# Kernel tuning notes

Hardware: AMD Instinct MI355X
Metric: run time of the kernel (lower is better)

The kernel has to match this reference:

```python
import jax, jax.numpy as jnp
import numpy as np

K = 20
EPS = 1e-5


def _knn_idx(x, k):
    # x: [B, N, D] -> indices of k nearest neighbors per node (self included,
    # matching torch_cluster.knn(x, x, k)).
    sq = jnp.sum(x * x, axis=-1)                      # [B, N]
    d = sq[:, :, None] + sq[:, None, :] - 2.0 * jnp.einsum('bnd,bmd->bnm', x, x)
    return jax.lax.top_k(-d, k)[1]                    # [B, N, k]


def _edge_feat(x, idx):
    # EdgeConv edge feature: concat(x_i, x_j - x_i)  -> [B, N, k, 2D]
    xj = jax.vmap(lambda xb, ib: xb[ib])(x, idx)      # [B, N, k, D]
    xi = jnp.broadcast_to(x[:, :, None, :], xj.shape)
    return jnp.concatenate([xi, xj - xi], axis=-1)


def _bn(h, g, b):
    # training-mode batch norm over all edges (PyG MLP default norm)
    mean = jnp.mean(h, axis=(0, 1, 2), keepdims=True)
    var = jnp.var(h, axis=(0, 1, 2), keepdims=True)
    return g * (h - mean) * jax.lax.rsqrt(var + EPS) + b


def _lin_init(key, fin, fout):
    k1, k2 = jax.random.split(key)
    s = 1.0 / np.sqrt(fin)
    W = jax.random.uniform(k1, (fin, fout), jnp.float32, -s, s)
    b = jax.random.uniform(k2, (fout,), jnp.float32, -s, s)
    return W, b


def setup_inputs() -> dict:
    key = jax.random.key(0)
    ks = jax.random.split(key, 8)
    B, N = 32, 1024
    pos = jax.random.normal(ks[0], (B, N, 3), jnp.float32)
    W1, b1 = _lin_init(ks[1], 6, 64)
    W2, b2 = _lin_init(ks[2], 64, 64)
    W3, b3 = _lin_init(ks[3], 64, 64)
    Wc2, bc2 = _lin_init(ks[4], 128, 128)
    Wl, bl = _lin_init(ks[5], 192, 1024)
    Wm1, bm1 = _lin_init(ks[6], 1024, 512)
    Wm2, bm2 = _lin_init(ks[7], 512, 256)
    Wm3, bm3 = _lin_init(jax.random.fold_in(key, 99), 256, 40)
    g1 = jnp.ones((64,), jnp.float32); be1 = jnp.zeros((64,), jnp.float32)
    g2 = jnp.ones((64,), jnp.float32); be2 = jnp.zeros((64,), jnp.float32)
    return dict(pos=pos, W1=W1, b1=b1, g1=g1, be1=be1, W2=W2, b2=b2, g2=g2,
                be2=be2, W3=W3, b3=b3, Wc2=Wc2, bc2=bc2, Wl=Wl, bl=bl,
                Wm1=Wm1, bm1=bm1, Wm2=Wm2, bm2=bm2, Wm3=Wm3, bm3=bm3)


def reference(pos, W1, b1, g1, be1, W2, b2, g2, be2, W3, b3, Wc2, bc2,
              Wl, bl, Wm1, bm1, Wm2, bm2, Wm3, bm3):
    # DynamicEdgeConv 1: kNN in coordinate space, MLP [6,64,64,64] (plain last)
    e1 = _edge_feat(pos, _knn_idx(pos, K))            # [B, N, k, 6]
    h = jax.nn.relu(_bn(e1 @ W1 + b1, g1, be1))
    h = jax.nn.relu(_bn(h @ W2 + b2, g2, be2))
    h = h @ W3 + b3
    x1 = jnp.max(h, axis=2)                           # [B, N, 64] max aggr
    # DynamicEdgeConv 2: kNN in feature space, single plain Linear 128->128
    e2 = _edge_feat(x1, _knn_idx(x1, K))              # [B, N, k, 128]
    x2 = jnp.max(e2 @ Wc2 + bc2, axis=2)              # [B, N, 128]
    # linear + global max pool + head MLP (norm=None, dropout=identity/eval)
    lin = jnp.concatenate([x1, x2], axis=-1) @ Wl + bl  # [B, N, 1024]
    pooled = jnp.max(lin, axis=1)                     # [B, 1024]
    h = jax.nn.relu(pooled @ Wm1 + bm1)
    h = jax.nn.relu(h @ Wm2 + bm2)
    return h @ Wm3 + bm3                              # [B, 40]
```

## Files before the change

### kernel.cpp

```cpp
#include <hip/hip_runtime.h>
#include <hip/hip_bf16.h>
#include <float.h>
#include <math.h>

typedef __hip_bfloat16 bf16;
typedef unsigned long long u64;

#define BATCH 32
#define NPTS  1024
#define KNN   20
#define NB    (BATCH*NPTS)
#define NEDGE (NB*KNN)

#define OFF_FLAG 512u
#define OFF_INB  1024u
#define OFF_IDX  988928u
#define OFF_X1   1644288u
#define OFF_X2   3741440u
#define OFF_C1   5838592u
#define OFF_POOL 7935744u
#define SLOW_END 8066816u
#define OFF_B2H  8066816u
#define FAST_END 10163968u
#define IN_POSF 0u
#define IN_B1   98304u
#define IN_G1   98368u
#define IN_BE1  98432u
#define IN_B2   98496u
#define IN_G2   98560u
#define IN_BE2  98624u
#define IN_B3   98688u
#define IN_BC2  98752u
#define IN_BL   98880u
#define IN_BM1  99904u
#define IN_BM2  100416u
#define IN_BM3  100672u
#define IN_W1   100736u
#define IN_WBUF 101120u
#define WB_W2   0u
#define WB_W3   4096u
#define WB_WD   8192u
#define WB_WBOT 16384u
#define WB_WL   24576u
#define WB_WM1  221184u
#define WB_WM2  745472u
#define WB_WM3  876544u
#define IN_TOTAL 987904u

__device__ __forceinline__ float bf2f(bf16 v){ return __bfloat162float(v); }

__device__ __forceinline__ unsigned int mono32(float f){
  unsigned int b = __float_as_uint(f);
  return b ^ ((unsigned int)((int)b >> 31) | 0x80000000u);
}

typedef __attribute__((ext_vector_type(8))) short bf16x8;
typedef __attribute__((ext_vector_type(4))) float f32x4;

__device__ __forceinline__ unsigned short bfhi(float f){
  unsigned int u = __float_as_uint(f);
  u += 0x7FFFu + ((u >> 16) & 1u);
  return (unsigned short)(u >> 16);
}
__device__ __forceinline__ void bfsplit(float f, unsigned short& h, unsigned short& l){
  h = bfhi(f);
  float fh = __uint_as_float(((unsigned int)h) << 16);
  l = bfhi(f - fh);
}

#define REP20(M) M(0) M(1) M(2) M(3) M(4) M(5) M(6) M(7) M(8) M(9) \
                 M(10) M(11) M(12) M(13) M(14) M(15) M(16) M(17) M(18) M(19)
#define SH19(M) M(19,18) M(18,17) M(17,16) M(16,15) M(15,14) M(14,13) M(13,12) \
                M(12,11) M(11,10) M(10,9) M(9,8) M(8,7) M(7,6) M(6,5) M(5,4) \
                M(4,3) M(3,2) M(2,1) M(1,0)

__device__ __forceinline__ double packkey(float d, int idx){
  unsigned int b = __float_as_uint(fmaxf(d, 0.0f));
  u64 k = 0x4000000000000000ULL | ((u64)b << 20) | (unsigned int)idx;
  return __longlong_as_double((long long)k);
}

#define KDECLD(p) double rk##p = DBL_MAX;
#define KMM(p,pm) rk##p = fmin(rk##p, fmax(rk##pm, _k));
#define INS_MM(kv) do{ double _k=(kv); SH19(KMM) rk0 = fmin(rk0, _k); }while(0)

#define KPUB_A(p) mrgA[q_l*21+p] = (u64)__double_as_longlong(rk##p);
#define KPUB_B(p) mrgB[q_l*21+p] = (u64)__double_as_longlong(rk##p);
#define KSTG(p)   gpart[p] = (u64)__double_as_longlong(rk##p);
#define KLDAD(p)  double rk##p = __longlong_as_double((long long)pa[p]);
#define KOUTU(p)  optr[p] = (int)((u64)__double_as_longlong(rk##p) & 1023ULL);

__global__ void k_sniff(const void* pos_raw, int* flag){
  if (blockIdx.x == 0 && threadIdx.x == 0){
    const unsigned short* h = (const unsigned short*)pos_raw;
    int wild = 0;
    for (int k = 0; k < 16; k++){
      unsigned int bits = ((unsigned int)h[2*k]) << 16;
      float v = __uint_as_float(bits);
      float a = fabsf(v);
      if (a != 0.0f && (v != v || a > 1e10f || a < 1e-10f)) wild++;
    }
    *flag = (wild >= 4) ? 1 : 0;
  }
}

__device__ __forceinline__ float rdv(const void* p, int i, int f){
  return f ? ((const float*)p)[i] : bf2f(((const bf16*)p)[i]);
}

__global__ __launch_bounds__(256) void k_cvt(
    const void* pos, const void* W1, const void* b1, const void* g1, const void* be1,
    const void* W2, const void* b2, const void* g2, const void* be2,
    const void* W3, const void* b3, const void* Wc2, const void* bc2,
    const void* Wl, const void* bl, const void* Wm1, const void* bm1,
    const void* Wm2, const void* bm2, const void* Wm3, const void* bm3,
    const int* flag, float* inb){
  int id = blockIdx.x*256 + threadIdx.x;
  if (id >= (int)IN_TOTAL) return;
  int f = *flag;
  float v;
  if      (id < 98304)  v = rdv(pos, id, f);
  else if (id < 98368)  v = rdv(b1,  id-98304, f);
  else if (id < 98432)  v = rdv(g1,  id-98368, f);
  else if (id < 98496)  v = rdv(be1, id-98432, f);
  else if (id < 98560)  v = rdv(b2,  id-98496, f);
  else if (id < 98624)  v = rdv(g2,  id-98560, f);
  else if (id < 98688)  v = rdv(be2, id-98624, f);
  else if (id < 98752)  v = rdv(b3,  id-98688, f);
  else if (id < 98880)  v = rdv(bc2, id-98752, f);
  else if (id < 99904)  v = rdv(bl,  id-98880, f);
  else if (id < 100416) v = rdv(bm1, id-99904, f);
  else if (id < 100672) v = rdv(bm2, id-100416, f);
  else if (id < 100712) v = rdv(bm3, id-100672, f);
  else if (id < 100736) v = 0.0f;
  else if (id < 101120) v = rdv(W1,  id-100736, f);
  else {
    int t = id - 101120;
    if      (t < 4096)   v = rdv(W2, t, f);
    else if (t < 8192)   v = rdv(W3, t-4096, f);
    else if (t < 16384){ int u = t-8192;  v = rdv(Wc2, u, f) - rdv(Wc2, 8192+u, f); }
    else if (t < 24576){ int u = t-16384; v = rdv(Wc2, 8192+u, f); }
    else if (t < 221184) v = rdv(Wl,  t-24576, f);
    else if (t < 745472){ int u = t-221184; int c = u>>10, d = u&1023; v = rdv(Wm1, d*512+c, f); }
    else if (t < 876544){ int u = t-745472; int c = u>>9,  d = u&511;  v = rdv(Wm2, d*256+c, f); }
    else               { int u = t-876544; int c = u>>8,  d = u&255;  v = rdv(Wm3, d*40+c, f); }
  }
  inb[id] = v;
}

__global__ __launch_bounds__(256) void k_prep1(const float* inb, float* a1, float* c1){
  const float* posf = inb + IN_POSF;
  const float* W1f  = inb + IN_W1;
  const float* b1f  = inb + IN_B1;
  int id = blockIdx.x*256 + threadIdx.x;
  int bn = id >> 6, c = id & 63;
  float p0 = posf[bn*3], p1 = posf[bn*3+1], p2 = posf[bn*3+2];
  float wt0 = W1f[c],     wt1 = W1f[64+c],  wt2 = W1f[128+c];
  float wb0 = W1f[192+c], wb1 = W1f[256+c], wb2 = W1f[320+c];
  float cv = p0*wb0 + p1*wb1 + p2*wb2;
  float av = p0*(wt0-wb0) + p1*(wt1-wb1) + p2*(wt2-wb2) + b1f[c];
  a1[id] = av;  c1[id] = cv;
}

__global__ __launch_bounds__(256, 2) void k_knn1(const float* inb, u64* part){
  const float* posf = inb + IN_POSF;
  __shared__ __align__(16) char sm1[21504];
  float* psx = (float*)sm1;
  float* psy = psx + 1024;
  float* psz = psy + 1024;
  float* sqs = psz + 1024;
  u64* mrgA = (u64*)sm1;
  u64* mrgB = (u64*)(sm1 + 10752);
  int bb   = blockIdx.x >> 5;
  int qg   = (blockIdx.x >> 1) & 15;
  int half = blockIdx.x & 1;
  int tid = threadIdx.x;
  int q_l = tid & 63;
  int slot = tid >> 6;
  for (int t = tid; t < 1024; t += 256){
    float x = posf[(bb*1024+t)*3], y = posf[(bb*1024+t)*3+1], z = posf[(bb*1024+t)*3+2];
    psx[t] = x; psy[t] = y; psz[t] = z; sqs[t] = x*x + y*y + z*z;
  }
  __syncthreads();
  int i_l = qg*64 + q_l;
  float xi0 = psx[i_l], xi1 = psy[i_l], xi2 = psz[i_l];
  float sqi = sqs[i_l];
  REP20(KDECLD)
  int cbase = half*512;
  for (int u = 0; u < 128; u++){
    int jj = cbase + 4*u + slot;
    float dot = xi0*psx[jj] + xi1*psy[jj] + xi2*psz[jj];
    float d = sqi + sqs[jj] - 2.0f*dot;
    INS_MM(packkey(d, jj));
  }
  __syncthreads();
  if (slot == 1){ REP20(KPUB_A) }
  if (slot == 3){ REP20(KPUB_B) }
  __syncthreads();
  if ((slot & 1) == 0){
    const u64* src = (slot == 0) ? &mrgA[q_l*21] : &mrgB[q_l*21];
    for (int p = 0; p < KNN; p++){
      double kv = __longlong_as_double((long long)src[p]);
      if (kv > rk19) break;
      INS_MM(kv);
    }
  }
  __syncthreads();
  if (slot == 2){ REP20(KPUB_B) }
  __syncthreads();
  if (slot == 0){
    const u64* src = &mrgB[q_l*21];
    for (int p = 0; p < KNN; p++){
      double kv = __longlong_as_double((long long)src[p]);
      if (kv > rk19) break;
      INS_MM(kv);
    }
    int gi = bb*1024 + i_l;
    u64* gpart = part + ((size_t)gi*2 + half)*KNN;
    REP20(KSTG)
  }
}

__global__ __launch_bounds__(256) void k_mrg(const u64* part, int* out){
  int gi = blockIdx.x*256 + threadIdx.x;
  const u64* pa = part + (size_t)gi*2*KNN;
  REP20(KLDAD)
  for (int p = 0; p < KNN; p++){
    double kv = __longlong_as_double((long long)pa[KNN + p]);
    if (kv > rk19) break;
    INS_MM(kv);
  }
  int* optr = out + gi*KNN;
  REP20(KOUTU)
}

__global__ __launch_bounds__(256) void k_stats1(const float* a1, const float* c1,
                                                const int* idx1, double* stats){
  __shared__ float rs[256], rs2[256];
  int tid = threadIdx.x, c = tid & 63, slot = tid >> 6;
  int base = blockIdx.x * 1024;
  float s = 0.f, s2 = 0.f;
  for (int t = 0; t < 256; t++){
    unsigned e = (unsigned)(base + t*4 + slot);
    int i = (int)(e / 20u);
    int b = i >> 10;
    int j = idx1[e];
    float h = a1[i*64+c] + c1[((b<<10)+j)*64 + c];
    s += h; s2 += h*h;
  }
  rs[tid] = s; rs2[tid] = s2;
  __syncthreads();
  if (slot == 0){
    double ts  = (double)rs[c]  + (double)rs[64+c]  + (double)rs[128+c]  + (double)rs[192+c];
    double ts2 = (double)rs2[c] + (double)rs2[64+c] + (double)rs2[128+c] + (double)rs2[192+c];
    atomicAdd(&stats[c], ts);
    atomicAdd(&stats[64+c], ts2);
  }
}


__global__ __launch_bounds__(256) void k_stats2m(const float* a1, const float* c1,
    const int* idx1, const float* inb, double* stats){
  __shared__ __align__(16) float W2s[4096];
  __shared__ float sc1s[64], sh1s[64];
  __shared__ float rs[4][64], rs2[4][64];
  int tid = threadIdx.x;
  const float* wbuf = inb + IN_WBUF;
  for (int t = tid; t < 4096; t += 256) W2s[t] = wbuf[WB_W2 + t];
  if (tid < 64){
    int c = tid;
    const double M = (double)NEDGE;
    double m1 = stats[c]/M;
    double v1 = stats[64+c]/M - m1*m1;
    double r1 = 1.0/sqrt(v1 + 1e-5);
    double g1 = (double)inb[IN_G1 + c];
    sc1s[c] = (float)(g1*r1);
    sh1s[c] = (float)((double)inb[IN_BE1 + c] - m1*g1*r1);
  }
  __syncthreads();
  int lane = tid & 63, wv = tid >> 6;
  int c16 = lane & 15, ag = lane >> 4, kb0 = ag*8;
  bf16x8 w2h[4][2], w2l[4][2];
  #pragma unroll
  for (int nt = 0; nt < 4; nt++){
    #pragma unroll
    for (int ks = 0; ks < 2; ks++){
      bf16x8 h8, l8;
      #pragma unroll
      for (int e = 0; e < 8; e++){
        unsigned short hh, ll;
        bfsplit(W2s[(ks*32 + kb0 + e)*64 + nt*16 + c16], hh, ll);
        h8[e] = (short)hh; l8[e] = (short)ll;
      }
      w2h[nt][ks] = h8; w2l[nt][ks] = l8;
    }
  }
  float sa[4] = {0,0,0,0}, qa[4] = {0,0,0,0};
  for (int t4 = 0; t4 < 4; t4++){
    int T = t4*4 + wv;
    int node_l = T >> 1, half = T & 1;
    int nodeg = blockIdx.x*8 + node_l;
    int krow = half*16 + c16;
    int rr = (krow < 20);
    int j = idx1[nodeg*20 + (rr ? krow : 0)];
    int gj = ((nodeg >> 10) << 10) + j;
    const float* ar = a1 + (size_t)nodeg*64;
    const float* cr = c1 + (size_t)gj*64;
    f32x4 av0 = *(const f32x4*)(ar + kb0);
    f32x4 av1 = *(const f32x4*)(ar + kb0 + 4);
    f32x4 av2 = *(const f32x4*)(ar + 32 + kb0);
    f32x4 av3 = *(const f32x4*)(ar + 36 + kb0);
    f32x4 cv0 = *(const f32x4*)(cr + kb0);
    f32x4 cv1 = *(const f32x4*)(cr + kb0 + 4);
    f32x4 cv2 = *(const f32x4*)(cr + 32 + kb0);
    f32x4 cv3 = *(const f32x4*)(cr + 36 + kb0);
    bf16x8 a0h, a0l, a1h_, a1l_;
    #pragma unroll
    for (int e = 0; e < 4; e++){
      unsigned short hh, ll;
      float h;
      h = rr ? fmaxf((av0[e]+cv0[e])*sc1s[kb0+e] + sh1s[kb0+e], 0.f) : 0.f;
      bfsplit(h, hh, ll); a0h[e] = (short)hh; a0l[e] = (short)ll;
      h = rr ? fmaxf((av1[e]+cv1[e])*sc1s[kb0+4+e] + sh1s[kb0+4+e], 0.f) : 0.f;
      bfsplit(h, hh, ll); a0h[4+e] = (short)hh; a0l[4+e] = (short)ll;
      h = rr ? fmaxf((av2[e]+cv2[e])*sc1s[32+kb0+e] + sh1s[32+kb0+e], 0.f) : 0.f;
      bfsplit(h, hh, ll); a1h_[e] = (short)hh; a1l_[e] = (short)ll;
      h = rr ? fmaxf((av3[e]+cv3[e])*sc1s[36+kb0+e] + sh1s[36+kb0+e], 0.f) : 0.f;
      bfsplit(h, hh, ll); a1h_[4+e] = (short)hh; a1l_[4+e] = (short)ll;
    }
    #pragma unroll
    for (int nt = 0; nt < 4; nt++){
      f32x4 acc = {0.f, 0.f, 0.f, 0.f};
      acc = __builtin_amdgcn_mfma_f32_16x16x32_bf16(a0h,  w2h[nt][0], acc, 0, 0, 0);
      acc = __builtin_amdgcn_mfma_f32_16x16x32_bf16(a1h_, w2h[nt][1], acc, 0, 0, 0);
      acc = __builtin_amdgcn_mfma_f32_16x16x32_bf16(a0h,  w2l[nt][0], acc, 0, 0, 0);
      acc = __builtin_amdgcn_mfma_f32_16x16x32_bf16(a1h_, w2l[nt][1], acc, 0, 0, 0);
      acc = __builtin_amdgcn_mfma_f32_16x16x32_bf16(a0l,  w2h[nt][0], acc, 0, 0, 0);
      acc = __builtin_amdgcn_mfma_f32_16x16x32_bf16(a1l_, w2h[nt][1], acc, 0, 0, 0);
      #pragma unroll
      for (int r = 0; r < 4; r++){
        int kr = half*16 + 4*ag + r;
        float v = (kr < 20) ? acc[r] : 0.f;
        sa[nt] += v; qa[nt] += v*v;
      }
    }
  }
  #pragma unroll
  for (int nt = 0; nt < 4; nt++){
    sa[nt] += __shfl_xor(sa[nt], 16); sa[nt] += __shfl_xor(sa[nt], 32);
    qa[nt] += __shfl_xor(qa[nt], 16); qa[nt] += __shfl_xor(qa[nt], 32);
  }
  if (ag == 0){
    #pragma unroll
    for (int nt = 0; nt < 4; nt++){
      rs[wv][nt*16+c16] = sa[nt];
      rs2[wv][nt*16+c16] = qa[nt];
    }
  }
  __syncthreads();
  if (tid < 64){
    double ts = (double)rs[0][tid] + (double)rs[1][tid]
              + (double)rs[2][tid] + (double)rs[3][tid];
    double tq = (double)rs2[0][tid] + (double)rs2[1][tid]
              + (double)rs2[2][tid] + (double)rs2[3][tid];
    atomicAdd(&stats[128+tid], ts);
    atomicAdd(&stats[192+tid], tq);
  }
}

__global__ __launch_bounds__(256, 2) void k_x1m(const float* a1, const float* c1,
    const int* idx1, const float* inb, const double* stats, float* x1){
  __shared__ __align__(16) unsigned short W2hF[4096], W2lF[4096];
  __shared__ __align__(16) unsigned short W3hF[4096], W3lF[4096];
  __shared__ __align__(16) float scr[4][16*68];
  __shared__ unsigned int mxp[4][8][64];
  __shared__ float sc1s[64], sh1s[64], sc2s[64], sh2s[64];
  int tid = threadIdx.x;
  const float* wbuf = inb + IN_WBUF;
  for (int t = tid; t < 4096; t += 256){
    int nt = t >> 10, ks = (t >> 9) & 1, ln = (t >> 3) & 63, e = t & 7;
    int row = ks*32 + (ln >> 4)*8 + e;
    int col = nt*16 + (ln & 15);
    unsigned short hh, ll;
    bfsplit(wbuf[WB_W2 + row*64 + col], hh, ll);
    W2hF[t] = hh; W2lF[t] = ll;
    bfsplit(wbuf[WB_W3 + row*64 + col], hh, ll);
    W3hF[t] = hh; W3lF[t] = ll;
  }
  {
    unsigned int* mf = &mxp[0][0][0];
    for (int t = tid; t < 2048; t += 256) mf[t] = 0u;
  }
  if (tid < 64){
    int c = tid;
    const double M = (double)NEDGE;
    double m1 = stats[c]/M;
    double v1 = stats[64+c]/M - m1*m1;
    double r1 = 1.0/sqrt(v1 + 1e-5);
    double g1 = (double)inb[IN_G1 + c];
    sc1s[c] = (float)(g1*r1);
    sh1s[c] = (float)((double)inb[IN_BE1 + c] - m1*g1*r1);
    double mp = stats[128+c]/M;
    double v2 = stats[192+c]/M - mp*mp;
    double r2 = 1.0/sqrt(v2 + 1e-5);
    double g2 = (double)inb[IN_G2 + c];
    sc2s[c] = (float)(g2*r2);
    sh2s[c] = (float)((double)inb[IN_BE2 + c] - mp*g2*r2);
  }
  __syncthreads();
  int lane = tid & 63, wv = tid >> 6;
  int c16 = lane & 15, ag = lane >> 4, kb0 = ag*8;
  float scn[4], shn[4];
  #pragma unroll
  for (int nt = 0; nt < 4; nt++){
    scn[nt] = sc2s[nt*16 + c16];
    shn[nt] = sh2s[nt*16 + c16];
  }
  float* sw = &scr[wv][0];
  for (int t4 = 0; t4 < 4; t4++){
    int T = t4*4 + wv;
    int node_l = T >> 1, half = T & 1;
    int nodeg = blockIdx.x*8 + node_l;
    int krow = half*16 + c16;
    int rr = (krow < 20);
    int j = idx1[nodeg*20 + (rr ? krow : 0)];
    int gj = ((nodeg >> 10) << 10) + j;
    const float* ar = a1 + (size_t)nodeg*64;
    const float* cr = c1 + (size_t)gj*64;
    f32x4 av0 = *(const f32x4*)(ar + kb0);
    f32x4 av1 = *(const f32x4*)(ar + kb0 + 4);
    f32x4 av2 = *(const f32x4*)(ar + 32 + kb0);
    f32x4 av3 = *(const f32x4*)(ar + 36 + kb0);
    f32x4 cv0 = *(const f32x4*)(cr + kb0);
    f32x4 cv1 = *(const f32x4*)(cr + kb0 + 4);
    f32x4 cv2 = *(const f32x4*)(cr + 32 + kb0);
    f32x4 cv3 = *(const f32x4*)(cr + 36 + kb0);
    bf16x8 a0h, a0l, a1h_, a1l_;
    #pragma unroll
    for (int e = 0; e < 4; e++){
      unsigned short hh, ll;
      float h;
      h = rr ? fmaxf((av0[e]+cv0[e])*sc1s[kb0+e] + sh1s[kb0+e], 0.f) : 0.f;
      bfsplit(h, hh, ll); a0h[e] = (short)hh; a0l[e] = (short)ll;
      h = rr ? fmaxf((av1[e]+cv1[e])*sc1s[kb0+4+e] + sh1s[kb0+4+e], 0.f) : 0.f;
      bfsplit(h, hh, ll); a0h[4+e] = (short)hh; a0l[4+e] = (short)ll;
      h = rr ? fmaxf((av2[e]+cv2[e])*sc1s[32+kb0+e] + sh1s[32+kb0+e], 0.f) : 0.f;
      bfsplit(h, hh, ll); a1h_[e] = (short)hh; a1l_[e] = (short)ll;
      h = rr ? fmaxf((av3[e]+cv3[e])*sc1s[36+kb0+e] + sh1s[36+kb0+e], 0.f) : 0.f;
      bfsplit(h, hh, ll); a1h_[4+e] = (short)hh; a1l_[4+e] = (short)ll;
    }
    f32x4 pacc[4];
    #pragma unroll
    for (int nt = 0; nt < 4; nt++){
      bf16x8 wh0 = *(const bf16x8*)(W2hF + (nt*2+0)*512 + lane*8);
      bf16x8 wh1 = *(const bf16x8*)(W2hF + (nt*2+1)*512 + lane*8);
      bf16x8 wl0 = *(const bf16x8*)(W2lF + (nt*2+0)*512 + lane*8);
      bf16x8 wl1 = *(const bf16x8*)(W2lF + (nt*2+1)*512 + lane*8);
      f32x4 acc = {0.f, 0.f, 0.f, 0.f};
      acc = __builtin_amdgcn_mfma_f32_16x16x32_bf16(a0h,  wh0, acc, 0, 0, 0);
      acc = __builtin_amdgcn_mfma_f32_16x16x32_bf16(a1h_, wh1, acc, 0, 0, 0);
      acc = __builtin_amdgcn_mfma_f32_16x16x32_bf16(a0h,  wl0, acc, 0, 0, 0);
      acc = __builtin_amdgcn_mfma_f32_16x16x32_bf16(a1h_, wl1, acc, 0, 0, 0);
      acc = __builtin_amdgcn_mfma_f32_16x16x32_bf16(a0l,  wh0, acc, 0, 0, 0);
      acc = __builtin_amdgcn_mfma_f32_16x16x32_bf16(a1l_, wh1, acc, 0, 0, 0);
      pacc[nt] = acc;
    }
    #pragma unroll
    for (int nt = 0; nt < 4; nt++){
      #pragma unroll
      for (int r = 0; r < 4; r++){
        float v = fmaxf(pacc[nt][r]*scn[nt] + shn[nt], 0.f);
        sw[(4*ag + r)*68 + nt*16 + c16] = v;
      }
    }
    f32x4 h20 = *(const f32x4*)(sw + c16*68 + kb0);
    f32x4 h21 = *(const f32x4*)(sw + c16*68 + kb0 + 4);
    f32x4 h22 = *(const f32x4*)(sw + c16*68 + 32 + kb0);
    f32x4 h23 = *(const f32x4*)(sw + c16*68 + 36 + kb0);
    bf16x8 b0h, b0l, b1h, b1l;
    #pragma unroll
    for (int e = 0; e < 4; e++){
      unsigned short hh, ll;
      bfsplit(h20[e], hh, ll); b0h[e] = (short)hh; b0l[e] = (short)ll;
      bfsplit(h21[e], hh, ll); b0h[4+e] = (short)hh; b0l[4+e] = (short)ll;
      bfsplit(h22[e], hh, ll); b1h[e] = (short)hh; b1l[e] = (short)ll;
      bfsplit(h23[e], hh, ll); b1h[4+e] = (short)hh; b1l[4+e] = (short)ll;
    }
    #pragma unroll
    for (int nt = 0; nt < 4; nt++){
      bf16x8 wh0 = *(const bf16x8*)(W3hF + (nt*2+0)*512 + lane*8);
      bf16x8 wh1 = *(const bf16x8*)(W3hF + (nt*2+1)*512 + lane*8);
      bf16x8 wl0 = *(const bf16x8*)(W3lF + (nt*2+0)*512 + lane*8);
      bf16x8 wl1 = *(const bf16x8*)(W3lF + (nt*2+1)*512 + lane*8);
      f32x4 acc = {0.f, 0.f, 0.f, 0.f};
      acc = __builtin_amdgcn_mfma_f32_16x16x32_bf16(b0h, wh0, acc, 0, 0, 0);
      acc = __builtin_amdgcn_mfma_f32_16x16x32_bf16(b1h, wh1, acc, 0, 0, 0);
      acc = __builtin_amdgcn_mfma_f32_16x16x32_bf16(b0h, wl0, acc, 0, 0, 0);
      acc = __builtin_amdgcn_mfma_f32_16x16x32_bf16(b1h, wl1, acc, 0, 0, 0);
      acc = __builtin_amdgcn_mfma_f32_16x16x32_bf16(b0l, wh0, acc, 0, 0, 0);
      acc = __builtin_amdgcn_mfma_f32_16x16x32_bf16(b1l, wh1, acc, 0, 0, 0);
      float vmx = -FLT_MAX;
      #pragma unroll
      for (int r = 0; r < 4; r++){
        int kr = half*16 + 4*ag + r;
        vmx = (kr < 20) ? fmaxf(vmx, acc[r]) : vmx;
      }
      vmx = fmaxf(vmx, __shfl_xor(vmx, 16));
      vmx = fmaxf(vmx, __shfl_xor(vmx, 32));
      if (ag == 0){
        unsigned int u = mono32(vmx);
        unsigned int* sl = &mxp[wv][node_l][nt*16 + c16];
        if (u > *sl) *sl = u;
      }
    }
  }
  __syncthreads();
  for (int s = tid; s < 512; s += 256){
    int nl = s >> 6, c = s & 63;
    unsigned int u = mxp[0][nl][c];
    unsigned int u1 = mxp[1][nl][c]; u = (u1 > u) ? u1 : u;
    unsigned int u2 = mxp[2][nl][c]; u = (u2 > u) ? u2 : u;
    unsigned int u3 = mxp[3][nl][c]; u = (u3 > u) ? u3 : u;
    unsigned int bts = (u & 0x80000000u) ? (u ^ 0x80000000u) : ~u;
    x1[(size_t)(blockIdx.x*8 + nl)*64 + c] = __uint_as_float(bts) + inb[IN_B3 + c];
  }
}

__global__ __launch_bounds__(256, 4) void k_knn2(const float* x1, u64* part){
  __shared__ __align__(16) char sm2[35584];
  unsigned short* Ch = (unsigned short*)sm2;
  unsigned short* Cl = (unsigned short*)(sm2 + 9216);
  float* Dd  = (float*)(sm2 + 18432);
  float* sqc = (float*)(sm2 + 35072);
  float* sqq = (float*)(sm2 + 35328);
  u64* mrgA = (u64*)sm2;
  u64* mrgB = (u64*)(sm2 + 10752);
  int bb   = blockIdx.x >> 5;
  int qg   = (blockIdx.x >> 1) & 15;
  int half = blockIdx.x & 1;
  int tid = threadIdx.x;
  int q_l = tid & 63;
  int wv = tid >> 6;
  int lane = tid & 63;
  int c16 = lane & 15, ag = lane >> 4, kb0 = ag*8;
  int qbase = bb*1024 + qg*64;
  bf16x8 qh0, qh1, ql0, ql1;
  {
    const float* qr = x1 + (size_t)(qbase + wv*16 + c16)*64;
    f32x4 v0 = *(const f32x4*)(qr + kb0);
    f32x4 v1 = *(const f32x4*)(qr + kb0 + 4);
    f32x4 v2 = *(const f32x4*)(qr + 32 + kb0);
    f32x4 v3 = *(const f32x4*)(qr + 36 + kb0);
    #pragma unroll
    for (int e = 0; e < 4; e++){
      unsigned short hh, ll;
      bfsplit(v0[e], hh, ll); qh0[e] = (short)hh; ql0[e] = (short)ll;
      bfsplit(v1[e], hh, ll); qh0[4+e] = (short)hh; ql0[4+e] = (short)ll;
      bfsplit(v2[e], hh, ll); qh1[e] = (short)hh; ql1[e] = (short)ll;
      bfsplit(v3[e], hh, ll); qh1[4+e] = (short)hh; ql1[4+e] = (short)ll;
    }
  }
  if (tid < 64){
    const float* xr = x1 + (size_t)(qbase + tid)*64;
    float s = 0.f;
    #pragma unroll
    for (int d4 = 0; d4 < 16; d4++){
      f32x4 v = *(const f32x4*)(xr + d4*4);
      s += v[0]*v[0] + v[1]*v[1] + v[2]*v[2] + v[3]*v[3];
    }
    sqq[tid] = s;
  }
  REP20(KDECLD)
  for (int ch = 0; ch < 8; ch++){
    int c0 = half*512 + ch*64;
    __syncthreads();
    for (int pp = tid; pp < 2048; pp += 256){
      int row = pp >> 5, cp = pp & 31;
      const float* src = x1 + (size_t)(bb*1024 + c0 + row)*64 + cp*2;
      float v0 = src[0], v1 = src[1];
      unsigned short h0, l0, h1, l1;
      bfsplit(v0, h0, l0); bfsplit(v1, h1, l1);
      ((unsigned int*)Ch)[row*36 + cp] = (unsigned int)h0 | ((unsigned int)h1 << 16);
      ((unsigned int*)Cl)[row*36 + cp] = (unsigned int)l0 | ((unsigned int)l1 << 16);
    }
    __syncthreads();
    if (tid < 64){
      float s = 0.f;
      for (int dw = 0; dw < 32; dw++){
        unsigned int hw = ((unsigned int*)Ch)[tid*36 + dw];
        unsigned int lw = ((unsigned int*)Cl)[tid*36 + dw];
        float a0 = __uint_as_float(hw << 16) + __uint_as_float(lw << 16);
        float a1 = __uint_as_float(hw & 0xFFFF0000u) + __uint_as_float(lw & 0xFFFF0000u);
        s += a0*a0 + a1*a1;
      }
      sqc[tid] = s;
    }
    __syncthreads();
    #pragma unroll
    for (int nt = 0; nt < 4; nt++){
      bf16x8 bh0 = *(const bf16x8*)(Ch + (nt*16 + c16)*72 + kb0);
      bf16x8 bh1 = *(const bf16x8*)(Ch + (nt*16 + c16)*72 + 32 + kb0);
      bf16x8 bl0 = *(const bf16x8*)(Cl + (nt*16 + c16)*72 + kb0);
      bf16x8 bl1 = *(const bf16x8*)(Cl + (nt*16 + c16)*72 + 32 + kb0);
      f32x4 p0 = {0.f,0.f,0.f,0.f}, p1 = {0.f,0.f,0.f,0.f}, p2 = {0.f,0.f,0.f,0.f};
      p0 = __builtin_amdgcn_mfma_f32_16x16x32_bf16(qh0, bh0, p0, 0, 0, 0);
      p0 = __builtin_amdgcn_mfma_f32_16x16x32_bf16(qh1, bh1, p0, 0, 0, 0);
      p1 = __builtin_amdgcn_mfma_f32_16x16x32_bf16(qh0, bl0, p1, 0, 0, 0);
      p1 = __builtin_amdgcn_mfma_f32_16x16x32_bf16(qh1, bl1, p1, 0, 0, 0);
      p2 = __builtin_amdgcn_mfma_f32_16x16x32_bf16(ql0, bh0, p2, 0, 0, 0);
      p2 = __builtin_amdgcn_mfma_f32_16x16x32_bf16(ql1, bh1, p2, 0, 0, 0);
      #pragma unroll
      for (int r = 0; r < 4; r++){
        int qrow = wv*16 + 4*ag + r;
        float d = sqq[qrow] + sqc[nt*16 + c16] - 2.0f*(p0[r] + p1[r] + p2[r]);
        Dd[qrow*65 + nt*16 + c16] = d;
      }
    }
    __syncthreads();
    for (int u = 0; u < 16; u += 2){
      int cA = 4*u + wv, cB = 4*(u+1) + wv;
      float dA = Dd[q_l*65 + cA];
      float dB = Dd[q_l*65 + cB];
      INS_MM(packkey(dA, c0 + cA));
      INS_MM(packkey(dB, c0 + cB));
    }
  }
  __syncthreads();
  if (wv == 1){ REP20(KPUB_A) }
  if (wv == 3){ REP20(KPUB_B) }
  __syncthreads();
  if ((wv & 1) == 0){
    const u64* src = (wv == 0) ? &mrgA[q_l*21] : &mrgB[q_l*21];
    for (int p = 0; p < KNN; p++){
      double kv = __longlong_as_double((long long)src[p]);
      if (kv > rk19) break;
      INS_MM(kv);
    }
  }
  __syncthreads();
  if (wv == 2){ REP20(KPUB_B) }
  __syncthreads();
  if (wv == 0){
    const u64* src = &mrgB[q_l*21];
    for (int p = 0; p < KNN; p++){
      double kv = __longlong_as_double((long long)src[p]);
      if (kv > rk19) break;
      INS_MM(kv);
    }
    int gi = qbase + q_l;
    u64* gpart = part + ((size_t)gi*2 + half)*KNN;
    REP20(KSTG)
  }
}

__global__ __launch_bounds__(256) void k_B2h(const float* x1, const float* inb,
                                             int q, float* B2H){
  __shared__ __align__(16) float Wbh[4096];
  __shared__ __align__(16) float xsh[1024];
  int tid = threadIdx.x;
  const float* Wb = inb + IN_WBUF + WB_WBOT;
  for (int t = tid; t < 4096; t += 256){
    int r = t >> 6, cl = t & 63;
    Wbh[t] = Wb[r*128 + q*64 + cl];
  }
  int node0 = blockIdx.x * 16;
  for (int t = tid; t < 1024; t += 256) xsh[t] = x1[node0*64 + t];
  __syncthreads();
  int n_l = tid >> 4, cg = tid & 15;
  const float* xr = xsh + n_l*64;
  float4 acc = make_float4(0.f,0.f,0.f,0.f);
  #pragma unroll 8
  for (int d = 0; d < 64; d++){
    float v = xr[d];
    float4 w = *(const float4*)(Wbh + d*64 + cg*4);
    acc.x += v*w.x; acc.y += v*w.y; acc.z += v*w.z; acc.w += v*w.w;
  }
  *(float4*)(B2H + (node0 + n_l)*64 + cg*4) = acc;
}

__global__ __launch_bounds__(256) void k_x2h(const float* x1, const float* B2H,
                                             const float* inb, const int* idx2,
                                             int q, float* x2){
  __shared__ __align__(16) float Wdh[4096];
  __shared__ __align__(16) float xsh[256];
  int tid = threadIdx.x;
  const float* Wd = inb + IN_WBUF + WB_WD;
  for (int t = tid; t < 4096; t += 256){
    int r = t >> 6, cl = t & 63;
    Wdh[t] = Wd[r*128 + q*64 + cl];
  }
  int node0 = blockIdx.x * 4;
  xsh[tid] = x1[node0*64 + tid];
  __syncthreads();
  int n_l = tid >> 6, cl = tid & 63;
  int i = node0 + n_l;
  int b = i >> 10;
  const float* xr = xsh + n_l*64;
  float acc = inb[IN_BC2 + q*64 + cl];
  #pragma unroll 8
  for (int d = 0; d < 64; d++) acc += xr[d]*Wdh[d*64 + cl];
  float m = -FLT_MAX;
  for (int kk = 0; kk < KNN; kk++){
    int j = idx2[i*KNN + kk];
    m = fmaxf(m, B2H[((b<<10)+j)*64 + cl]);
  }
  x2[i*128 + q*64 + cl] = acc + m;
}

__global__ __launch_bounds__(256) void k_x2d(const float* x1, const float* inb,
                                             const int* idx2, float* x2){
  __shared__ __align__(16) float Wdh[4096], Wbh[4096];
  __shared__ __align__(16) float xis[1024], xjs[1024];
  int tid = threadIdx.x;
  int q = blockIdx.x & 1;
  int node0 = (blockIdx.x >> 1) * 16;
  const float* Wd = inb + IN_WBUF + WB_WD;
  const float* Wb = inb + IN_WBUF + WB_WBOT;
  for (int t = tid; t < 4096; t += 256){
    int r = t >> 6, cl = t & 63;
    Wdh[t] = Wd[r*128 + q*64 + cl];
    Wbh[t] = Wb[r*128 + q*64 + cl];
  }
  for (int t = tid; t < 1024; t += 256) xis[t] = x1[node0*64 + t];
  __syncthreads();
  int n_l = tid >> 4, cg = tid & 15;
  int i = node0 + n_l, b = i >> 10;
  const float* xr = xis + n_l*64;
  float4 af = make_float4(inb[IN_BC2 + q*64 + cg*4],   inb[IN_BC2 + q*64 + cg*4+1],
                          inb[IN_BC2 + q*64 + cg*4+2], inb[IN_BC2 + q*64 + cg*4+3]);
  #pragma unroll 8
  for (int d = 0; d < 64; d++){
    float v = xr[d];
    float4 w = *(const float4*)(Wdh + d*64 + cg*4);
    af.x += v*w.x; af.y += v*w.y; af.z += v*w.z; af.w += v*w.w;
  }
  float4 mx = make_float4(-FLT_MAX,-FLT_MAX,-FLT_MAX,-FLT_MAX);
  for (int kk = 0; kk < KNN; kk++){
    __syncthreads();
    for (int t = tid; t < 1024; t += 256){
      int nn = t >> 6, r = t & 63;
      int jj = idx2[(node0+nn)*KNN + kk];
      xjs[t] = x1[((((node0+nn) >> 10) << 10) + jj)*64 + r];
    }
    __syncthreads();
    const float* xj = xjs + n_l*64;
    float4 acc = make_float4(0.f,0.f,0.f,0.f);
    #pragma unroll 8
    for (int d = 0; d < 64; d++){
      float v = xj[d];
      float4 w = *(const float4*)(Wbh + d*64 + cg*4);
      acc.x += v*w.x; acc.y += v*w.y; acc.z += v*w.z; acc.w += v*w.w;
    }
    mx.x = fmaxf(mx.x, acc.x); mx.y = fmaxf(mx.y, acc.y);
    mx.z = fmaxf(mx.z, acc.z); mx.w = fmaxf(mx.w, acc.w);
  }
  *(float4*)(x2 + i*128 + q*64 + cg*4) =
      make_float4(af.x+mx.x, af.y+mx.y, af.z+mx.z, af.w+mx.w);
}

__global__ __launch_bounds__(512, 2) void k_linpoolm(const float* x1, const float* x2,
    const float* inb, float* pool4){
  __shared__ __align__(16) float F[16*196];
  int tid = threadIdx.x;
  int b = blockIdx.x >> 4, cq = (blockIdx.x >> 2) & 3, nh = blockIdx.x & 3;
  int lane = tid & 63, wv = tid >> 6;
  int c16 = lane & 15, ag = lane >> 4;
  const float* Wl = inb + IN_WBUF + WB_WL;
  bf16x8 w_h[2][6], w_l[2][6];
  #pragma unroll
  for (int nt = 0; nt < 2; nt++){
    int col = cq*256 + (wv*2+nt)*16 + c16;
    #pragma unroll
    for (int ks = 0; ks < 6; ks++){
      bf16x8 h8, l8;
      #pragma unroll
      for (int e = 0; e < 8; e++){
        unsigned short hh, ll;
        bfsplit(Wl[(ks*32 + ag*8 + e)*1024 + col], hh, ll);
        h8[e] = (short)hh; l8[e] = (short)ll;
      }
      w_h[nt][ks] = h8; w_l[nt][ks] = l8;
    }
  }
  float rmax[2] = {-FLT_MAX, -FLT_MAX};
  int n0 = b*1024 + nh*256;
  for (int chk = 0; chk < 16; chk++){
    int nb = n0 + chk*16;
    __syncthreads();
    {
      int row = tid >> 5;
      int d0 = (tid & 31)*6;
      #pragma unroll
      for (int u = 0; u < 6; u++){
        int d = d0 + u;
        F[row*196 + d] = (d < 64) ? x1[(size_t)(nb+row)*64 + d]
                                  : x2[(size_t)(nb+row)*128 + d - 64];
      }
    }
    __syncthreads();
    bf16x8 a_h[6], a_l[6];
    #pragma unroll
    for (int ks = 0; ks < 6; ks++){
      f32x4 v0 = *(const f32x4*)(F + c16*196 + ks*32 + ag*8);
      f32x4 v1 = *(const f32x4*)(F + c16*196 + ks*32 + ag*8 + 4);
      bf16x8 h8, l8;
      #pragma unroll
      for (int e = 0; e < 4; e++){
        unsigned short hh, ll;
        bfsplit(v0[e], hh, ll); h8[e] = (short)hh; l8[e] = (short)ll;
        bfsplit(v1[e], hh, ll); h8[4+e] = (short)hh; l8[4+e] = (short)ll;
      }
      a_h[ks] = h8; a_l[ks] = l8;
    }
    #pragma unroll
    for (int nt = 0; nt < 2; nt++){
      f32x4 p0 = {0.f,0.f,0.f,0.f}, p1 = {0.f,0.f,0.f,0.f}, p2 = {0.f,0.f,0.f,0.f};
      #pragma unroll
      for (int ks = 0; ks < 6; ks++){
        p0 = __builtin_amdgcn_mfma_f32_16x16x32_bf16(a_h[ks], w_h[nt][ks], p0, 0, 0, 0);
        p1 = __builtin_amdgcn_mfma_f32_16x16x32_bf16(a_h[ks], w_l[nt][ks], p1, 0, 0, 0);
        p2 = __builtin_amdgcn_mfma_f32_16x16x32_bf16(a_l[ks], w_h[nt][ks], p2, 0, 0, 0);
      }
      float m = -FLT_MAX;
      #pragma unroll
      for (int r = 0; r < 4; r++) m = fmaxf(m, p0[r] + p1[r] + p2[r]);
// ... 143 lines not shown
```

Measured before the change: 820.9 us.

## Pack edges densely into MFMA tiles to drop padded rows in stats2 and x1

Each node previously had 20 edges spread over two 16-row MFMA tiles, so 12 of every 32 rows were padding. The kernels now pack a block's 160 edges contiguously into 10 full 16-row tiles, with tiles that straddle two nodes split into two max reductions merged by shared-memory atomicMax. stats2m also stops building the W2 hi/lo fragments in registers and reads pre-split fragments from shared memory, as x1m already did. This cuts MFMA and gather work by about a fifth, at the cost of idle waves in the last round (10 tiles over 4 waves) and LDS atomics.

```diff
diff --git a/kernel.cpp b/kernel.cpp
--- a/kernel.cpp
+++ b/kernel.cpp
@@ -261,12 +261,19 @@
 
 __global__ __launch_bounds__(256) void k_stats2m(const float* a1, const float* c1,
     const int* idx1, const float* inb, double* stats){
-  __shared__ __align__(16) float W2s[4096];
+  __shared__ __align__(16) unsigned short W2hF[4096], W2lF[4096];
   __shared__ float sc1s[64], sh1s[64];
   __shared__ float rs[4][64], rs2[4][64];
   int tid = threadIdx.x;
   const float* wbuf = inb + IN_WBUF;
-  for (int t = tid; t < 4096; t += 256) W2s[t] = wbuf[WB_W2 + t];
+  for (int t = tid; t < 4096; t += 256){
+    int nt = t >> 10, ks = (t >> 9) & 1, ln = (t >> 3) & 63, e = t & 7;
+    int row = ks*32 + (ln >> 4)*8 + e;
+    int col = nt*16 + (ln & 15);
+    unsigned short hh, ll;
+    bfsplit(wbuf[WB_W2 + row*64 + col], hh, ll);
+    W2hF[t] = hh; W2lF[t] = ll;
+  }
   if (tid < 64){
     int c = tid;
     const double M = (double)NEDGE;
@@ -280,68 +287,57 @@
   __syncthreads();
   int lane = tid & 63, wv = tid >> 6;
   int c16 = lane & 15, ag = lane >> 4, kb0 = ag*8;
-  bf16x8 w2h[4][2], w2l[4][2];
-  #pragma unroll
-  for (int nt = 0; nt < 4; nt++){
-    #pragma unroll
-    for (int ks = 0; ks < 2; ks++){
-      bf16x8 h8, l8;
-      #pragma unroll
-      for (int e = 0; e < 8; e++){
+  float sa[4] = {0,0,0,0}, qa[4] = {0,0,0,0};
+  for (int rd = 0; rd < 3; rd++){
+    int T = rd*4 + wv;
+    if (T < 10){
+      int krow = 16*T + c16;
+      int node = (krow*52429) >> 20;
+      int nodeg = blockIdx.x*8 + node;
+      int j = idx1[blockIdx.x*160 + krow];
+      int gj = ((nodeg >> 10) << 10) + j;
+      const float* ar = a1 + (size_t)nodeg*64;
+      const float* cr = c1 + (size_t)gj*64;
+      f32x4 av0 = *(const f32x4*)(ar + kb0);
+      f32x4 av1 = *(const f32x4*)(ar + kb0 + 4);
+      f32x4 av2 = *(const f32x4*)(ar + 32 + kb0);
+      f32x4 av3 = *(const f32x4*)(ar + 36 + kb0);
+      f32x4 cv0 = *(const f32x4*)(cr + kb0);
+      f32x4 cv1 = *(const f32x4*)(cr + kb0 + 4);
+      f32x4 cv2 = *(const f32x4*)(cr + 32 + kb0);
+      f32x4 cv3 = *(const f32x4*)(cr + 36 + kb0);
+      bf16x8 a0h, a0l, a1h_, a1l_;
+      #pragma unroll
+      for (int e = 0; e < 4; e++){
         unsigned short hh, ll;
-        bfsplit(W2s[(ks*32 + kb0 + e)*64 + nt*16 + c16], hh, ll);
-        h8[e] = (short)hh; l8[e] = (short)ll;
-      }
-      w2h[nt][ks] = h8; w2l[nt][ks] = l8;
-    }
-  }
-  float sa[4] = {0,0,0,0}, qa[4] = {0,0,0,0};
-  for (int t4 = 0; t4 < 4; t4++){
-    int T = t4*4 + wv;
-    int node_l = T >> 1, half = T & 1;
-    int nodeg = blockIdx.x*8 + node_l;
-    int krow = half*16 + c16;
-    int rr = (krow < 20);
-    int j = idx1[nodeg*20 + (rr ? krow : 0)];
-    int gj = ((nodeg >> 10) << 10) + j;
-    const float* ar = a1 + (size_t)nodeg*64;
-    const float* cr = c1 + (size_t)gj*64;
-    f32x4 av0 = *(const f32x4*)(ar + kb0);
-    f32x4 av1 = *(const f32x4*)(ar + kb0 + 4);
-    f32x4 av2 = *(const f32x4*)(ar + 32 + kb0);
-    f32x4 av3 = *(const f32x4*)(ar + 36 + kb0);
-    f32x4 cv0 = *(const f32x4*)(cr + kb0);
-    f32x4 cv1 = *(const f32x4*)(cr + kb0 + 4);
-    f32x4 cv2 = *(const f32x4*)(cr + 32 + kb0);
-    f32x4 cv3 = *(const f32x4*)(cr + 36 + kb0);
-    bf16x8 a0h, a0l, a1h_, a1l_;
-    #pragma unroll
-    for (int e = 0; e < 4; e++){
-      unsigned short hh, ll;
-      float h;
-      h = rr ? fmaxf((av0[e]+cv0[e])*sc1s[kb0+e] + sh1s[kb0+e], 0.f) : 0.f;
-      bfsplit(h, hh, ll); a0h[e] = (short)hh; a0l[e] = (short)ll;
-      h = rr ? fmaxf((av1[e]+cv1[e])*sc1s[kb0+4+e] + sh1s[kb0+4+e], 0.f) : 0.f;
-      bfsplit(h, hh, ll); a0h[4+e] = (short)hh; a0l[4+e] = (short)ll;
-      h = rr ? fmaxf((av2[e]+cv2[e])*sc1s[32+kb0+e] + sh1s[32+kb0+e], 0.f) : 0.f;
-      bfsplit(h, hh, ll); a1h_[e] = (short)hh; a1l_[e] = (short)ll;
-      h = rr ? fmaxf((av3[e]+cv3[e])*sc1s[36+kb0+e] + sh1s[36+kb0+e], 0.f) : 0.f;
-      bfsplit(h, hh, ll); a1h_[4+e] = (short)hh; a1l_[4+e] = (short)ll;
-    }
-    #pragma unroll
-    for (int nt = 0; nt < 4; nt++){
-      f32x4 acc = {0.f, 0.f, 0.f, 0.f};
-      acc = __builtin_amdgcn_mfma_f32_16x16x32_bf16(a0h,  w2h[nt][0], acc, 0, 0, 0);
-      acc = __builtin_amdgcn_mfma_f32_16x16x32_bf16(a1h_, w2h[nt][1], acc, 0, 0, 0);
-      acc = __builtin_amdgcn_mfma_f32_16x16x32_bf16(a0h,  w2l[nt][0], acc, 0, 0, 0);
-      acc = __builtin_amdgcn_mfma_f32_16x16x32_bf16(a1h_, w2l[nt][1], acc, 0, 0, 0);
-      acc = __builtin_amdgcn_mfma_f32_16x16x32_bf16(a0l,  w2h[nt][0], acc, 0, 0, 0);
-      acc = __builtin_amdgcn_mfma_f32_16x16x32_bf16(a1l_, w2h[nt][1], acc, 0, 0, 0);
-      #pragma unroll
-      for (int r = 0; r < 4; r++){
-        int kr = half*16 + 4*ag + r;
-        float v = (kr < 20) ? acc[r] : 0.f;
-        sa[nt] += v; qa[nt] += v*v;
+        float h;
+        h = fmaxf((av0[e]+cv0[e])*sc1s[kb0+e] + sh1s[kb0+e], 0.f);
+        bfsplit(h, hh, ll); a0h[e] = (short)hh; a0l[e] = (short)ll;
+        h = fmaxf((av1[e]+cv1[e])*sc1s[kb0+4+e] + sh1s[kb0+4+e], 0.f);
+        bfsplit(h, hh, ll); a0h[4+e] = (short)hh; a0l[4+e] = (short)ll;
+        h = fmaxf((av2[e]+cv2[e])*sc1s[32+kb0+e] + sh1s[32+kb0+e], 0.f);
+        bfsplit(h, hh, ll); a1h_[e] = (short)hh; a1l_[e] = (short)ll;
+        h = fmaxf((av3[e]+cv3[e])*sc1s[36+kb0+e] + sh1s[36+kb0+e], 0.f);
+        bfsplit(h, hh, ll); a1h_[4+e] = (short)hh; a1l_[4+e] = (short)ll;
+      }
+      #pragma unroll
+      for (int nt = 0; nt < 4; nt++){
+        bf16x8 wh0 = *(const bf16x8*)(W2hF + (nt*2+0)*512 + lane*8);
+        bf16x8 wh1 = *(const bf16x8*)(W2hF + (nt*2+1)*512 + lane*8);
+        bf16x8 wl0 = *(const bf16x8*)(W2lF + (nt*2+0)*512 + lane*8);
+        bf16x8 wl1 = *(const bf16x8*)(W2lF + (nt*2+1)*512 + lane*8);
+        f32x4 acc = {0.f, 0.f, 0.f, 0.f};
+        acc = __builtin_amdgcn_mfma_f32_16x16x32_bf16(a0h,  wh0, acc, 0, 0, 0);
+        acc = __builtin_amdgcn_mfma_f32_16x16x32_bf16(a1h_, wh1, acc, 0, 0, 0);
+        acc = __builtin_amdgcn_mfma_f32_16x16x32_bf16(a0h,  wl0, acc, 0, 0, 0);
+        acc = __builtin_amdgcn_mfma_f32_16x16x32_bf16(a1h_, wl1, acc, 0, 0, 0);
+        acc = __builtin_amdgcn_mfma_f32_16x16x32_bf16(a0l,  wh0, acc, 0, 0, 0);
+        acc = __builtin_amdgcn_mfma_f32_16x16x32_bf16(a1l_, wh1, acc, 0, 0, 0);
+        #pragma unroll
+        for (int r = 0; r < 4; r++){
+          float v = acc[r];
+          sa[nt] += v; qa[nt] += v*v;
+        }
       }
     }
   }
@@ -373,7 +369,7 @@
   __shared__ __align__(16) unsigned short W2hF[4096], W2lF[4096];
   __shared__ __align__(16) unsigned short W3hF[4096], W3lF[4096];
   __shared__ __align__(16) float scr[4][16*68];
-  __shared__ unsigned int mxp[4][8][64];
+  __shared__ unsigned int mxp2[8][64];
   __shared__ float sc1s[64], sh1s[64], sc2s[64], sh2s[64];
   int tid = threadIdx.x;
   const float* wbuf = inb + IN_WBUF;
@@ -387,10 +383,7 @@
     bfsplit(wbuf[WB_W3 + row*64 + col], hh, ll);
     W3hF[t] = hh; W3lF[t] = ll;
   }
-  {
-    unsigned int* mf = &mxp[0][0][0];
-    for (int t = tid; t < 2048; t += 256) mf[t] = 0u;
-  }
+  for (int t = tid; t < 512; t += 256) ((unsigned int*)mxp2)[t] = 0u;
   if (tid < 64){
     int c = tid;
     const double M = (double)NEDGE;
@@ -417,110 +410,116 @@
     shn[nt] = sh2s[nt*16 + c16];
   }
   float* sw = &scr[wv][0];
-  for (int t4 = 0; t4 < 4; t4++){
-    int T = t4*4 + wv;
-    int node_l = T >> 1, half = T & 1;
-    int nodeg = blockIdx.x*8 + node_l;
-    int krow = half*16 + c16;
-    int rr = (krow < 20);
-    int j = idx1[nodeg*20 + (rr ? krow : 0)];
-    int gj = ((nodeg >> 10) << 10) + j;
-    const float* ar = a1 + (size_t)nodeg*64;
-    const float* cr = c1 + (size_t)gj*64;
-    f32x4 av0 = *(const f32x4*)(ar + kb0);
-    f32x4 av1 = *(const f32x4*)(ar + kb0 + 4);
-    f32x4 av2 = *(const f32x4*)(ar + 32 + kb0);
-    f32x4 av3 = *(const f32x4*)(ar + 36 + kb0);
-    f32x4 cv0 = *(const f32x4*)(cr + kb0);
-    f32x4 cv1 = *(const f32x4*)(cr + kb0 + 4);
-    f32x4 cv2 = *(const f32x4*)(cr + 32 + kb0);
-    f32x4 cv3 = *(const f32x4*)(cr + 36 + kb0);
-    bf16x8 a0h, a0l, a1h_, a1l_;
-    #pragma unroll
-    for (int e = 0; e < 4; e++){
-      unsigned short hh, ll;
-      float h;
-      h = rr ? fmaxf((av0[e]+cv0[e])*sc1s[kb0+e] + sh1s[kb0+e], 0.f) : 0.f;
-      bfsplit(h, hh, ll); a0h[e] = (short)hh; a0l[e] = (short)ll;
-      h = rr ? fmaxf((av1[e]+cv1[e])*sc1s[kb0+4+e] + sh1s[kb0+4+e], 0.f) : 0.f;
-      bfsplit(h, hh, ll); a0h[4+e] = (short)hh; a0l[4+e] = (short)ll;
-      h = rr ? fmaxf((av2[e]+cv2[e])*sc1s[32+kb0+e] + sh1s[32+kb0+e], 0.f) : 0.f;
-      bfsplit(h, hh, ll); a1h_[e] = (short)hh; a1l_[e] = (short)ll;
-      h = rr ? fmaxf((av3[e]+cv3[e])*sc1s[36+kb0+e] + sh1s[36+kb0+e], 0.f) : 0.f;
-      bfsplit(h, hh, ll); a1h_[4+e] = (short)hh; a1l_[4+e] = (short)ll;
-    }
-    f32x4 pacc[4];
-    #pragma unroll
-    for (int nt = 0; nt < 4; nt++){
-      bf16x8 wh0 = *(const bf16x8*)(W2hF + (nt*2+0)*512 + lane*8);
-      bf16x8 wh1 = *(const bf16x8*)(W2hF + (nt*2+1)*512 + lane*8);
-      bf16x8 wl0 = *(const bf16x8*)(W2lF + (nt*2+0)*512 + lane*8);
-      bf16x8 wl1 = *(const bf16x8*)(W2lF + (nt*2+1)*512 + lane*8);
-      f32x4 acc = {0.f, 0.f, 0.f, 0.f};
-      acc = __builtin_amdgcn_mfma_f32_16x16x32_bf16(a0h,  wh0, acc, 0, 0, 0);
-      acc = __builtin_amdgcn_mfma_f32_16x16x32_bf16(a1h_, wh1, acc, 0, 0, 0);
-      acc = __builtin_amdgcn_mfma_f32_16x16x32_bf16(a0h,  wl0, acc, 0, 0, 0);
-      acc = __builtin_amdgcn_mfma_f32_16x16x32_bf16(a1h_, wl1, acc, 0, 0, 0);
-      acc = __builtin_amdgcn_mfma_f32_16x16x32_bf16(a0l,  wh0, acc, 0, 0, 0);
-      acc = __builtin_amdgcn_mfma_f32_16x16x32_bf16(a1l_, wh1, acc, 0, 0, 0);
-      pacc[nt] = acc;
-    }
-    #pragma unroll
-    for (int nt = 0; nt < 4; nt++){
-      #pragma unroll
-      for (int r = 0; r < 4; r++){
-        float v = fmaxf(pacc[nt][r]*scn[nt] + shn[nt], 0.f);
-        sw[(4*ag + r)*68 + nt*16 + c16] = v;
-      }
-    }
-    f32x4 h20 = *(const f32x4*)(sw + c16*68 + kb0);
-    f32x4 h21 = *(const f32x4*)(sw + c16*68 + kb0 + 4);
-    f32x4 h22 = *(const f32x4*)(sw + c16*68 + 32 + kb0);
-    f32x4 h23 = *(const f32x4*)(sw + c16*68 + 36 + kb0);
-    bf16x8 b0h, b0l, b1h, b1l;
-    #pragma unroll
-    for (int e = 0; e < 4; e++){
-      unsigned short hh, ll;
-      bfsplit(h20[e], hh, ll); b0h[e] = (short)hh; b0l[e] = (short)ll;
-      bfsplit(h21[e], hh, ll); b0h[4+e] = (short)hh; b0l[4+e] = (short)ll;
-      bfsplit(h22[e], hh, ll); b1h[e] = (short)hh; b1l[e] = (short)ll;
-      bfsplit(h23[e], hh, ll); b1h[4+e] = (short)hh; b1l[4+e] = (short)ll;
-    }
-    #pragma unroll
-    for (int nt = 0; nt < 4; nt++){
-      bf16x8 wh0 = *(const bf16x8*)(W3hF + (nt*2+0)*512 + lane*8);
-      bf16x8 wh1 = *(const bf16x8*)(W3hF + (nt*2+1)*512 + lane*8);
-      bf16x8 wl0 = *(const bf16x8*)(W3lF + (nt*2+0)*512 + lane*8);
-      bf16x8 wl1 = *(const bf16x8*)(W3lF + (nt*2+1)*512 + lane*8);
-      f32x4 acc = {0.f, 0.f, 0.f, 0.f};
-      acc = __builtin_amdgcn_mfma_f32_16x16x32_bf16(b0h, wh0, acc, 0, 0, 0);
-      acc = __builtin_amdgcn_mfma_f32_16x16x32_bf16(b1h, wh1, acc, 0, 0, 0);
-      acc = __builtin_amdgcn_mfma_f32_16x16x32_bf16(b0h, wl0, acc, 0, 0, 0);
-      acc = __builtin_amdgcn_mfma_f32_16x16x32_bf16(b1h, wl1, acc, 0, 0, 0);
-      acc = __builtin_amdgcn_mfma_f32_16x16x32_bf16(b0l, wh0, acc, 0, 0, 0);
-      acc = __builtin_amdgcn_mfma_f32_16x16x32_bf16(b1l, wh1, acc, 0, 0, 0);
-      float vmx = -FLT_MAX;
-      #pragma unroll
-      for (int r = 0; r < 4; r++){
-        int kr = half*16 + 4*ag + r;
-        vmx = (kr < 20) ? fmaxf(vmx, acc[r]) : vmx;
-      }
-      vmx = fmaxf(vmx, __shfl_xor(vmx, 16));
-      vmx = fmaxf(vmx, __shfl_xor(vmx, 32));
-      if (ag == 0){
-        unsigned int u = mono32(vmx);
-        unsigned int* sl = &mxp[wv][node_l][nt*16 + c16];
-        if (u > *sl) *sl = u;
+  for (int rd = 0; rd < 3; rd++){
+    int T = rd*4 + wv;
+    if (T < 10){
+      int krow = 16*T + c16;
+      int node = (krow*52429) >> 20;
+      int nodeg = blockIdx.x*8 + node;
+      int j = idx1[blockIdx.x*160 + krow];
+      int gj = ((nodeg >> 10) << 10) + j;
+      const float* ar = a1 + (size_t)nodeg*64;
+      const float* cr = c1 + (size_t)gj*64;
+      f32x4 av0 = *(const f32x4*)(ar + kb0);
+      f32x4 av1 = *(const f32x4*)(ar + kb0 + 4);
+      f32x4 av2 = *(const f32x4*)(ar + 32 + kb0);
+      f32x4 av3 = *(const f32x4*)(ar + 36 + kb0);
+      f32x4 cv0 = *(const f32x4*)(cr + kb0);
+      f32x4 cv1 = *(const f32x4*)(cr + kb0 + 4);
+      f32x4 cv2 = *(const f32x4*)(cr + 32 + kb0);
+      f32x4 cv3 = *(const f32x4*)(cr + 36 + kb0);
+      bf16x8 a0h, a0l, a1h_, a1l_;
+      #pragma unroll
+      for (int e = 0; e < 4; e++){
+        unsigned short hh, ll;
+        float h;
+        h = fmaxf((av0[e]+cv0[e])*sc1s[kb0+e] + sh1s[kb0+e], 0.f);
+        bfsplit(h, hh, ll); a0h[e] = (short)hh; a0l[e] = (short)ll;
+        h = fmaxf((av1[e]+cv1[e])*sc1s[kb0+4+e] + sh1s[kb0+4+e], 0.f);
+        bfsplit(h, hh, ll); a0h[4+e] = (short)hh; a0l[4+e] = (short)ll;
+        h = fmaxf((av2[e]+cv2[e])*sc1s[32+kb0+e] + sh1s[32+kb0+e], 0.f);
+        bfsplit(h, hh, ll); a1h_[e] = (short)hh; a1l_[e] = (short)ll;
+        h = fmaxf((av3[e]+cv3[e])*sc1s[36+kb0+e] + sh1s[36+kb0+e], 0.f);
+        bfsplit(h, hh, ll); a1h_[4+e] = (short)hh; a1l_[4+e] = (short)ll;
+      }
+      f32x4 pacc[4];
+      #pragma unroll
+      for (int nt = 0; nt < 4; nt++){
+        bf16x8 wh0 = *(const bf16x8*)(W2hF + (nt*2+0)*512 + lane*8);
+        bf16x8 wh1 = *(const bf16x8*)(W2hF + (nt*2+1)*512 + lane*8);
+        bf16x8 wl0 = *(const bf16x8*)(W2lF + (nt*2+0)*512 + lane*8);
+        bf16x8 wl1 = *(const bf16x8*)(W2lF + (nt*2+1)*512 + lane*8);
+        f32x4 acc = {0.f, 0.f, 0.f, 0.f};
+        acc = __builtin_amdgcn_mfma_f32_16x16x32_bf16(a0h,  wh0, acc, 0, 0, 0);
+        acc = __builtin_amdgcn_mfma_f32_16x16x32_bf16(a1h_, wh1, acc, 0, 0, 0);
+        acc = __builtin_amdgcn_mfma_f32_16x16x32_bf16(a0h,  wl0, acc, 0, 0, 0);
+        acc = __builtin_amdgcn_mfma_f32_16x16x32_bf16(a1h_, wl1, acc, 0, 0, 0);
+        acc = __builtin_amdgcn_mfma_f32_16x16x32_bf16(a0l,  wh0, acc, 0, 0, 0);
+        acc = __builtin_amdgcn_mfma_f32_16x16x32_bf16(a1l_, wh1, acc, 0, 0, 0);
+        pacc[nt] = acc;
+      }
+      #pragma unroll
+      for (int nt = 0; nt < 4; nt++){
+        #pragma unroll
+        for (int r = 0; r < 4; r++){
+          float v = fmaxf(pacc[nt][r]*scn[nt] + shn[nt], 0.f);
+          sw[(4*ag + r)*68 + nt*16 + c16] = v;
+        }
+      }
+      f32x4 h20 = *(const f32x4*)(sw + c16*68 + kb0);
+      f32x4 h21 = *(const f32x4*)(sw + c16*68 + kb0 + 4);
+      f32x4 h22 = *(const f32x4*)(sw + c16*68 + 32 + kb0);
+      f32x4 h23 = *(const f32x4*)(sw + c16*68 + 36 + kb0);
+      bf16x8 b0h, b0l, b1h, b1l;
+      #pragma unroll
+      for (int e = 0; e < 4; e++){
+        unsigned short hh, ll;
+        bfsplit(h20[e], hh, ll); b0h[e] = (short)hh; b0l[e] = (short)ll;
+        bfsplit(h21[e], hh, ll); b0h[4+e] = (short)hh; b0l[4+e] = (short)ll;
+        bfsplit(h22[e], hh, ll); b1h[e] = (short)hh; b1l[e] = (short)ll;
+        bfsplit(h23[e], hh, ll); b1h[4+e] = (short)hh; b1l[4+e] = (short)ll;
+      }
+      int rowA = 16*T;
+      int nA = (rowA*52429) >> 20;
+      int bnd = nA*20 + 20 - rowA;
+      int hasB = (bnd < 16);
+      #pragma unroll
+      for (int nt = 0; nt < 4; nt++){
+        bf16x8 wh0 = *(const bf16x8*)(W3hF + (nt*2+0)*512 + lane*8);
+        bf16x8 wh1 = *(const bf16x8*)(W3hF + (nt*2+1)*512 + lane*8);
+        bf16x8 wl0 = *(const bf16x8*)(W3lF + (nt*2+0)*512 + lane*8);
+        bf16x8 wl1 = *(const bf16x8*)(W3lF + (nt*2+1)*512 + lane*8);
+        f32x4 acc = {0.f, 0.f, 0.f, 0.f};
+        acc = __builtin_amdgcn_mfma_f32_16x16x32_bf16(b0h, wh0, acc, 0, 0, 0);
+        acc = __builtin_amdgcn_mfma_f32_16x16x32_bf16(b1h, wh1, acc, 0, 0, 0);
+        acc = __builtin_amdgcn_mfma_f32_16x16x32_bf16(b0h, wl0, acc, 0, 0, 0);
+        acc = __builtin_amdgcn_mfma_f32_16x16x32_bf16(b1h, wl1, acc, 0, 0, 0);
+        acc = __builtin_amdgcn_mfma_f32_16x16x32_bf16(b0l, wh0, acc, 0, 0, 0);
+        acc = __builtin_amdgcn_mfma_f32_16x16x32_bf16(b1l, wh1, acc, 0, 0, 0);
+        float mA = -FLT_MAX, mB = -FLT_MAX;
+        #pragma unroll
+        for (int r = 0; r < 4; r++){
+          int rw = 4*ag + r;
+          float v = acc[r];
+          bool inA = (rw < bnd);
+          mA = inA ? fmaxf(mA, v) : mA;
+          mB = inA ? mB : fmaxf(mB, v);
+        }
+        mA = fmaxf(mA, __shfl_xor(mA, 16));
+        mA = fmaxf(mA, __shfl_xor(mA, 32));
+        mB = fmaxf(mB, __shfl_xor(mB, 16));
+        mB = fmaxf(mB, __shfl_xor(mB, 32));
+        if (ag == 0){
+          atomicMax(&mxp2[nA][nt*16 + c16], mono32(mA));
+          if (hasB) atomicMax(&mxp2[nA+1][nt*16 + c16], mono32(mB));
+        }
       }
     }
   }
   __syncthreads();
   for (int s = tid; s < 512; s += 256){
     int nl = s >> 6, c = s & 63;
-    unsigned int u = mxp[0][nl][c];
-    unsigned int u1 = mxp[1][nl][c]; u = (u1 > u) ? u1 : u;
-    unsigned int u2 = mxp[2][nl][c]; u = (u2 > u) ? u2 : u;
-    unsigned int u3 = mxp[3][nl][c]; u = (u3 > u) ? u3 : u;
+    unsigned int u = mxp2[nl][c];
     unsigned int bts = (u & 0x80000000u) ? (u ^ 0x80000000u) : ~u;
     x1[(size_t)(blockIdx.x*8 + nl)*64 + c] = __uint_as_float(bts) + inb[IN_B3 + c];
   }
```

After: 762.3 us (median of 2 runs). -7.1%, faster.
